# Performance work log

Hardware: AMD Instinct MI355X
Metric: run time of the kernel (lower is better)

## Reference

```python
import jax, jax.numpy as jnp
import numpy as np

B, T, N, D = 2, 10, 1024, 1024
NH = 16
HD = D // NH


def setup_inputs() -> dict:
    key = jax.random.key(0)
    ks = jax.random.split(key, 9)
    data = jax.random.normal(ks[0], (B, N, D), jnp.float32)
    traj_pos = jax.random.normal(ks[1], (B, T, N, 3), jnp.float32)
    q = jax.random.normal(ks[2], (B, T, N, 4), jnp.float32)
    traj_quat = q / (jnp.linalg.norm(q, axis=-1, keepdims=True) + 1e-10)
    certainty = jax.random.uniform(ks[3], (B, N), jnp.float32)
    s = 1.0 / np.sqrt(D).astype(np.float32)
    Wq = jax.random.normal(ks[4], (D, D), jnp.float32) * s
    Wk = jax.random.normal(ks[5], (D, D), jnp.float32) * s
    Wv = jax.random.normal(ks[6], (D, D), jnp.float32) * s
    Wo = jax.random.normal(ks[7], (D, D), jnp.float32) * s
    z = jnp.zeros((D,), jnp.float32)
    return {"data": data, "traj_pos": traj_pos, "traj_quat": traj_quat,
            "certainty": certainty, "Wq": Wq, "bq": z, "Wk": Wk, "bk": z,
            "Wv": Wv, "bv": z, "Wo": Wo, "bo": z}


def reference(data, traj_pos, traj_quat, certainty, Wq, bq, Wk, bk, Wv, bv, Wo, bo):
    b, n, d = data.shape
    # --- trajectory similarity scores (same for all batches: torch.mean over batch+time) ---
    # pos_dist[i,j] = mean_{b,t} ||p_bti - p_btj||
    pd = jnp.linalg.norm(traj_pos[:, :, :, None, :] - traj_pos[:, :, None, :, :], axis=-1).mean(axis=(0, 1))  # (n,n)
    qdm = jnp.linalg.norm(traj_quat[:, :, :, None, :] - traj_quat[:, :, None, :, :], axis=-1).mean(axis=(0, 1))
    qdp = jnp.linalg.norm(traj_quat[:, :, :, None, :] + traj_quat[:, :, None, :, :], axis=-1).mean(axis=(0, 1))
    qd = jnp.minimum(qdm, qdp)
    traj = jnp.exp(-pd - qd)
    traj = traj / traj.sum(axis=-1, keepdims=True)  # (n,n) row-normalized

    def proj(x, W, bias):
        return (x @ W.T + bias).reshape(b, n, NH, HD).transpose(0, 2, 1, 3)  # (b,h,n,hd)

    Q = proj(data, Wq, bq)
    K = proj(data, Wk, bk)
    V = proj(data, Wv, bv)
    scores = jnp.einsum('bhid,bhjd->bhij', Q, K) / np.sqrt(HD).astype(np.float32)
    combined = scores + 0.5 * traj[None, None]  # broadcast over (batch, heads)
    attn = jax.nn.softmax(combined, axis=-1)
    out = jnp.einsum('bhij,bhjd->bhid', attn, V).transpose(0, 2, 1, 3).reshape(b, n, d)
    out = out @ Wo.T + bo
    # certainty update from attention entropy
    avg_attn = attn.mean(axis=1)  # (b,n,n)
    p = jnp.clip(avg_attn, 1e-10, None)
    Hent = -jnp.sum(p * jnp.log(p), axis=-1)  # (b,n)
    H_max = np.log(n).astype(np.float32)
    new_certainty = jnp.maximum(certainty, jax.nn.sigmoid(H_max - Hent))
    return out, new_certainty
```

## Files before the change

### kernel.cpp

```cpp
#include <hip/hip_runtime.h>
#include <math.h>

#define NB 2
#define NN 1024
#define DD 1024
#define NHH 16
#define HDD 64
#define BTT 20

typedef unsigned short u16;
typedef short bf16x8 __attribute__((ext_vector_type(8)));
typedef float f32x4 __attribute__((ext_vector_type(4)));

#define HMAXL 6.93147180559945f
#define LN2 0.69314718055994531f
#define C1 0.18033688011112042f
#define TLC 0.72134752044448170f
#define KC  0.072134752044448170f
#define CH 520

#define TRAJ_OFF 0
#define TL_OFF    1048576
#define DATAB_OFF 1572864
#define WQB_OFF   2621440
#define WKB_OFF   3145728
#define WVB_OFF   3670016
#define WOB_OFF   4194304
#define QB_OFF    4718592
#define KB_OFF    5767168
#define VT_OFF    6815744
#define AOB_OFF   7864320
#define LV_OFF    8912896
#define RSP_OFF   8978432
#define EB_OFF    8982528

__device__ __forceinline__ float b2f(u16 h) { return __uint_as_float(((unsigned)h) << 16); }
__device__ __forceinline__ u16 f2bf(float f) {
  unsigned u = __float_as_uint(f);
  return (u16)((u + 0x7fffu + ((u >> 16) & 1u)) >> 16);
}
__device__ __forceinline__ unsigned pkbf(float a, float b) {
  unsigned r;
  asm("v_cvt_pk_bf16_f32 %0, %1, %2" : "=v"(r) : "v"(a), "v"(b));
  return r;
}
__device__ __forceinline__ void dma16(const void* g, void* l) {
  __builtin_amdgcn_global_load_lds((const __attribute__((address_space(1))) void*)g,
                                   (__attribute__((address_space(3))) void*)l, 16, 0, 0);
}

__global__ __launch_bounds__(256) void prep_kernel(const float* __restrict__ data,
                                                   const float* __restrict__ w0,
                                                   const float* __restrict__ w1,
                                                   const float* __restrict__ w2,
                                                   const float* __restrict__ w3,
                                                   u16* __restrict__ dd,
                                                   u16* __restrict__ d0, u16* __restrict__ d1,
                                                   u16* __restrict__ d2, u16* __restrict__ d3,
                                                   const float* __restrict__ pos,
                                                   const float* __restrict__ quat,
                                                   float* __restrict__ w,
                                                   float* __restrict__ rsp) {
  const int tid = threadIdx.x;
  const int bid = blockIdx.x;
  __shared__ float ld[8][BTT][8];
  __shared__ float wredS[4][8];
  if (bid >= 512) {
    int cb = bid - 512;
    int z = cb >> 10;
    const float* s;
    u16* d;
    size_t off = 0;
    if (z < 2) { s = data; d = dd; off = (size_t)z * 1048576; }
    else if (z == 2) { s = w0; d = d0; }
    else if (z == 3) { s = w1; d = d1; }
    else if (z == 4) { s = w2; d = d2; }
    else { s = w3; d = d3; }
    size_t i = off + (size_t)((cb & 1023) * 256 + tid) * 4;
    float4 v = *(const float4*)(s + i);
    ushort4 o = {f2bf(v.x), f2bf(v.y), f2bf(v.z), f2bf(v.w)};
    *(ushort4*)(d + i) = o;
    return;
  }
  const int jx = bid & 3;
  const int j = jx * 256 + tid;
  const int i0 = (bid >> 2) * 8;
  if (tid < 8 * BTT) {
    int ii = tid / BTT, bt = tid % BTT;
    const float* pp = pos + ((size_t)bt * NN + i0 + ii) * 3;
    ld[ii][bt][0] = pp[0]; ld[ii][bt][1] = pp[1]; ld[ii][bt][2] = pp[2];
    *(float4*)&ld[ii][bt][4] = *(const float4*)(quat + ((size_t)bt * NN + i0 + ii) * 4);
  }
  __syncthreads();
  float acc[8] = {};
  for (int bt = 0; bt < BTT; ++bt) {
    const float* pj = pos + ((size_t)bt * NN + j) * 3;
    float pjx = pj[0], pjy = pj[1], pjz = pj[2];
    float4 qj = *(const float4*)(quat + ((size_t)bt * NN + j) * 4);
#pragma unroll
    for (int ii = 0; ii < 8; ++ii) {
      float4 pi = *(const float4*)&ld[ii][bt][0];
      float4 qi = *(const float4*)&ld[ii][bt][4];
      float dx = pi.x - pjx, dy = pi.y - pjy, dz = pi.z - pjz;
      float d2 = fmaf(dz, dz, fmaf(dy, dy, dx * dx));
      float dot = fmaf(qi.w, qj.w, fmaf(qi.z, qj.z, fmaf(qi.y, qj.y, qi.x * qj.x)));
      float tq = fmaf(-2.f, fabsf(dot), 2.f);
      acc[ii] += sqrtf(d2) + sqrtf(fmaxf(tq, 0.f));
    }
  }
  const int wv = tid >> 6;
#pragma unroll
  for (int ii = 0; ii < 8; ++ii) {
    float v = exp2f(-acc[ii] * KC);
    w[(size_t)(i0 + ii) * NN + j] = v;
    float s = v;
#pragma unroll
    for (int off = 1; off < 64; off <<= 1) s += __shfl_xor(s, off, 64);
    if ((tid & 63) == 0) wredS[wv][ii] = s;
  }
  __syncthreads();
  if (tid < 8)
    rsp[jx * 1024 + i0 + tid] = wredS[0][tid] + wredS[1][tid] + wredS[2][tid] + wredS[3][tid];
}

__global__ __launch_bounds__(256, 3) void qkv_trajB_kernel(const u16* __restrict__ Ab,
                                                        const u16* __restrict__ Wq,
                                                        const u16* __restrict__ Wk,
                                                        const u16* __restrict__ Wv,
                                                        const float* __restrict__ bq,
                                                        const float* __restrict__ bk,
                                                        const float* __restrict__ bv,
                                                        u16* __restrict__ Qb,
                                                        u16* __restrict__ Kb,
                                                        u16* __restrict__ VtT,
                                                        const float* __restrict__ wtr,
                                                        const float* __restrict__ rsp,
                                                        u16* __restrict__ tl) {
  const int tid = threadIdx.x;
  __shared__ __align__(16) u16 As[128 * 64];
  __shared__ __align__(16) u16 Bs[2][64 * 64];
  if (blockIdx.x < 256) {
    int base = blockIdx.x * 4;
#pragma unroll
    for (int r = 0; r < 4; ++r) {
      int i = base + r;
      float inv = TLC / (rsp[i] + rsp[1024 + i] + rsp[2048 + i] + rsp[3072 + i]);
      float4 w4 = *(const float4*)(wtr + (size_t)i * NN + tid * 4);
      ushort4 o = {f2bf(w4.x * inv), f2bf(w4.y * inv), f2bf(w4.z * inv), f2bf(w4.w * inv)};
      *(ushort4*)(tl + (size_t)i * NN + tid * 4) = o;
    }
    return;
  }
  const int bid = blockIdx.x - 256;
  const bool isQK = bid < 256;
  const int rem = bid & 255;
  const int bn = (rem & 15) << 6;
  const int bm = (rem >> 4) << 7;
  const int w = tid >> 6, l = tid & 63, g = l >> 4, ln = l & 15;
  const int lr = l >> 3;
  const int sgc = ((l & 7) ^ lr) * 8;
  const u16* ApA = Ab + (size_t)(bm + w * 32 + lr) * DD + sgc;
  u16* dAc = As + (w * 4) * 512;
  const int mw = (w & 1) * 64, nw = (w >> 1) * 32;
  const int lx = ln & 7;
  f32x4 zero4 = {0.f, 0.f, 0.f, 0.f};
  if (isQK) {
    const u16* BqP = Wq + (size_t)(bn + w * 16 + lr) * DD + sgc;
    const u16* BkP = Wk + (size_t)(bn + w * 16 + lr) * DD + sgc;
    u16* dBq = Bs[0] + (w * 2) * 512;
    u16* dBk = Bs[1] + (w * 2) * 512;
    f32x4 acc[2][4][2];
#pragma unroll
    for (int z = 0; z < 2; ++z)
#pragma unroll
      for (int mt = 0; mt < 4; ++mt)
#pragma unroll
        for (int nt = 0; nt < 2; ++nt) acc[z][mt][nt] = zero4;
    for (int k0 = 0; k0 < DD; k0 += 64) {
      __syncthreads();
#pragma unroll
      for (int d = 0; d < 4; ++d)
        dma16(ApA + (size_t)(d * 8) * DD + k0, dAc + d * 512);
#pragma unroll
      for (int d = 0; d < 2; ++d) {
        dma16(BqP + (size_t)(d * 8) * DD + k0, dBq + d * 512);
        dma16(BkP + (size_t)(d * 8) * DD + k0, dBk + d * 512);
      }
      __syncthreads();
#pragma unroll
      for (int kc = 0; kc < 2; ++kc) {
        const int so = ((kc * 4 + g) ^ lx) * 8;
        bf16x8 afr[4], bqf[2], bkf[2];
#pragma unroll
        for (int nt = 0; nt < 2; ++nt) {
          int off = (nw + nt * 16 + ln) * 64 + so;
          bqf[nt] = *(const bf16x8*)&Bs[0][off];
          bkf[nt] = *(const bf16x8*)&Bs[1][off];
        }
#pragma unroll
        for (int mt = 0; mt < 4; ++mt)
          afr[mt] = *(const bf16x8*)&As[(mw + mt * 16 + ln) * 64 + so];
#pragma unroll
        for (int mt = 0; mt < 4; ++mt)
#pragma unroll
          for (int nt = 0; nt < 2; ++nt) {
            acc[0][mt][nt] = __builtin_amdgcn_mfma_f32_16x16x32_bf16(afr[mt], bqf[nt], acc[0][mt][nt], 0, 0, 0);
            acc[1][mt][nt] = __builtin_amdgcn_mfma_f32_16x16x32_bf16(afr[mt], bkf[nt], acc[1][mt][nt], 0, 0, 0);
          }
      }
    }
#pragma unroll
    for (int z = 0; z < 2; ++z) {
      u16* outp = z == 0 ? Qb : Kb;
      const float* bias = z == 0 ? bq : bk;
#pragma unroll
      for (int nt = 0; nt < 2; ++nt) {
        int n = bn + nw + nt * 16 + ln;
        float bb = bias[n];
#pragma unroll
        for (int mt = 0; mt < 4; ++mt) {
#pragma unroll
          for (int r = 0; r < 4; ++r) {
            int m = bm + mw + mt * 16 + g * 4 + r;
            outp[(size_t)m * DD + n] = f2bf(acc[z][mt][nt][r] + bb);
          }
        }
      }
    }
    return;
  }
  const u16* BvP = Wv + (size_t)(bn + w * 16 + lr) * DD + sgc;
  u16* dBv = Bs[0] + (w * 2) * 512;
  f32x4 acc[4][2];
#pragma unroll
  for (int mt = 0; mt < 4; ++mt)
#pragma unroll
    for (int nt = 0; nt < 2; ++nt) acc[mt][nt] = zero4;
  for (int k0 = 0; k0 < DD; k0 += 64) {
    __syncthreads();
#pragma unroll
    for (int d = 0; d < 4; ++d)
      dma16(ApA + (size_t)(d * 8) * DD + k0, dAc + d * 512);
#pragma unroll
    for (int d = 0; d < 2; ++d)
      dma16(BvP + (size_t)(d * 8) * DD + k0, dBv + d * 512);
    __syncthreads();
#pragma unroll
    for (int kc = 0; kc < 2; ++kc) {
      const int so = ((kc * 4 + g) ^ lx) * 8;
      bf16x8 bfr[2], afr[4];
#pragma unroll
      for (int nt = 0; nt < 2; ++nt)
        bfr[nt] = *(const bf16x8*)&Bs[0][(nw + nt * 16 + ln) * 64 + so];
#pragma unroll
      for (int mt = 0; mt < 4; ++mt)
        afr[mt] = *(const bf16x8*)&As[(mw + mt * 16 + ln) * 64 + so];
#pragma unroll
      for (int mt = 0; mt < 4; ++mt)
#pragma unroll
        for (int nt = 0; nt < 2; ++nt)
          acc[mt][nt] = __builtin_amdgcn_mfma_f32_16x16x32_bf16(afr[mt], bfr[nt], acc[mt][nt], 0, 0, 0);
    }
  }
#pragma unroll
  for (int nt = 0; nt < 2; ++nt) {
    int n = bn + nw + nt * 16 + ln;
    float bb = bv[n];
    int row = (((bm >> 10) << 4) + (n >> 6)) * 64 + (n & 63);
#pragma unroll
    for (int mt = 0; mt < 4; ++mt) {
      int tok = (bm & 1023) + mw + mt * 16 + g * 4;
      ushort4 pk = {f2bf(acc[mt][nt][0] + bb), f2bf(acc[mt][nt][1] + bb),
                    f2bf(acc[mt][nt][2] + bb), f2bf(acc[mt][nt][3] + bb)};
      *(ushort4*)(VtT + (size_t)row * NN + tok) = pk;
    }
  }
}

__global__ __launch_bounds__(256) void att_kernel(const u16* __restrict__ Qb,
                                                  const u16* __restrict__ Kb,
                                                  const u16* __restrict__ VtT,
                                                  const u16* __restrict__ tl,
                                                  u16* __restrict__ AOb,
                                                  float* __restrict__ Lv,
                                                  u16* __restrict__ Eb) {
  const int tid = threadIdx.x;
  const int bh = blockIdx.y;
  const int b = bh >> 4, h = bh & 15;
  const int i0 = blockIdx.x << 6;
  const int w = tid >> 6, l = tid & 63, g = l >> 4, ln = l & 15;
  const int wi0 = w * 16;
  __shared__ __align__(16) u16 Qs[8 * CH];
  __shared__ __align__(16) u16 Ks[2][8 * CH];
  __shared__ __align__(16) u16 Vts[2][8 * CH];
  __shared__ __align__(16) u16 Pt[64 * 72];
  __shared__ float lsc[64];
  const int c0 = 2 * w, c1 = 2 * w + 1;
  const int rr = 8 * (l >> 3);
  const int dcol = (l & 7) * 8;
  dma16(Qb + ((size_t)(b * NN) + i0 + c0 + rr) * DD + h * HDD + dcol, Qs + c0 * CH);
  dma16(Qb + ((size_t)(b * NN) + i0 + c1 + rr) * DD + h * HDD + dcol, Qs + c1 * CH);
  const int ig = i0 + wi0 + ln;
  u16* Erow = Eb + ((size_t)bh * NN + ig) * NN;
  const int lnlo = (ln & 7) * CH;
  const int lnhi = (ln >> 3) * 64;
  f32x4 zero4 = {0.f, 0.f, 0.f, 0.f};
  f32x4 oacc[4];
#pragma unroll
  for (int nt = 0; nt < 4; ++nt) oacc[nt] = zero4;
  float lacc = 0.f;
  for (int j0 = 0; j0 < NN; j0 += 128) {
    __syncthreads();
#pragma unroll
    for (int u = 0; u < 2; ++u) {
      int jb = j0 + u * 64;
      dma16(Kb + ((size_t)(b * NN) + jb + c0 + rr) * DD + h * HDD + dcol, Ks[u] + c0 * CH);
      dma16(Kb + ((size_t)(b * NN) + jb + c1 + rr) * DD + h * HDD + dcol, Ks[u] + c1 * CH);
      dma16(VtT + ((size_t)(bh * 64) + c0 + rr) * NN + jb + dcol, Vts[u] + c0 * CH);
      dma16(VtT + ((size_t)(bh * 64) + c1 + rr) * NN + jb + dcol, Vts[u] + c1 * CH);
    }
    ushort4 tlv[2][4];
#pragma unroll
    for (int u = 0; u < 2; ++u)
#pragma unroll
      for (int jt = 0; jt < 4; ++jt)
        tlv[u][jt] = *(const ushort4*)(tl + (size_t)ig * NN + j0 + u * 64 + jt * 16 + g * 4);
    __syncthreads();
    bf16x8 qf[2];
    qf[0] = *(const bf16x8*)&Qs[lnlo + (2 * w) * 64 + lnhi + g * 8];
    qf[1] = *(const bf16x8*)&Qs[lnlo + (2 * w) * 64 + lnhi + 32 + g * 8];
#pragma unroll
    for (int u = 0; u < 2; ++u) {
      f32x4 sacc[4];
      __builtin_amdgcn_s_setprio(1);
#pragma unroll
      for (int jt = 0; jt < 4; ++jt) {
        sacc[jt] = zero4;
#pragma unroll
        for (int kc = 0; kc < 2; ++kc) {
          bf16x8 af = *(const bf16x8*)&Ks[u][lnlo + (2 * jt) * 64 + lnhi + kc * 32 + g * 8];
          sacc[jt] = __builtin_amdgcn_mfma_f32_16x16x32_bf16(af, qf[kc], sacc[jt], 0, 0, 0);
        }
      }
      __builtin_amdgcn_s_setprio(0);
#pragma unroll
      for (int jt = 0; jt < 4; ++jt) {
        float e0 = exp2f(sacc[jt][0] * C1 + b2f(tlv[u][jt].x));
        float e1 = exp2f(sacc[jt][1] * C1 + b2f(tlv[u][jt].y));
        float e2 = exp2f(sacc[jt][2] * C1 + b2f(tlv[u][jt].z));
        float e3 = exp2f(sacc[jt][3] * C1 + b2f(tlv[u][jt].w));
        lacc += (e0 + e1) + (e2 + e3);
        uint2 pk = {pkbf(e0, e1), pkbf(e2, e3)};
        *(uint2*)(Pt + (wi0 + ln) * 72 + jt * 16 + g * 4) = pk;
        *(uint2*)(Erow + j0 + u * 64 + jt * 16 + g * 4) = pk;
      }
      bf16x8 pf[2];
      pf[0] = *(const bf16x8*)&Pt[(wi0 + ln) * 72 + g * 8];
      pf[1] = *(const bf16x8*)&Pt[(wi0 + ln) * 72 + 32 + g * 8];
      __builtin_amdgcn_s_setprio(1);
#pragma unroll
      for (int nt = 0; nt < 4; ++nt) {
#pragma unroll
        for (int kc = 0; kc < 2; ++kc) {
          bf16x8 vf = *(const bf16x8*)&Vts[u][lnlo + (2 * nt) * 64 + lnhi + kc * 32 + g * 8];
          oacc[nt] = __builtin_amdgcn_mfma_f32_16x16x32_bf16(pf[kc], vf, oacc[nt], 0, 0, 0);
        }
      }
      __builtin_amdgcn_s_setprio(0);
    }
  }
  lacc += __shfl_xor(lacc, 16, 64);
  lacc += __shfl_xor(lacc, 32, 64);
  if (g == 0) {
    Lv[(size_t)bh * NN + i0 + wi0 + ln] = lacc;
    lsc[wi0 + ln] = 1.f / lacc;
  }
  __syncthreads();
#pragma unroll
  for (int nt = 0; nt < 4; ++nt) {
    int d = nt * 16 + ln;
#pragma unroll
    for (int r = 0; r < 4; ++r) {
      int i = wi0 + g * 4 + r;
      float v = oacc[nt][r] * lsc[i];
      AOb[((size_t)(b * NN) + i0 + i) * DD + h * HDD + d] = f2bf(v);
    }
  }
}

__global__ __launch_bounds__(256) void gemmo_ent_kernel(const u16* __restrict__ Ab,
                                                        const u16* __restrict__ Wb,
                                                        const float* __restrict__ bias,
                                                        float* __restrict__ C,
                                                        const u16* __restrict__ Eb,
                                                        const float* __restrict__ Lv,
                                                        const float* __restrict__ cert,
                                                        float* __restrict__ outc) {
  const int tid = threadIdx.x;
  __shared__ __align__(16) u16 As[128 * 64];
  __shared__ __align__(16) u16 Bs[64 * 64];
  __shared__ float linvS[4][16];
  __shared__ float redS[4][4];
  if (blockIdx.x >= 256) {
    const int e = blockIdx.x - 256;
    const int b = e >> 8;
    const int ib4 = (e & 255) << 2;
    if (tid < 64) {
      int r = tid >> 4, h = tid & 15;
      linvS[r][h] = 1.f / Lv[((size_t)(b * 16 + h)) * NN + ib4 + r];
    }
    __syncthreads();
    const int jb = tid * 4;
    float A[4];
#pragma unroll
    for (int r = 0; r < 4; ++r) {
      float s0 = 0.f, s1 = 0.f, s2 = 0.f, s3 = 0.f;
#pragma unroll
      for (int h = 0; h < 16; ++h) {
        ushort4 v = *(const ushort4*)(Eb + (((size_t)(b * 16 + h)) * NN + ib4 + r) * NN + jb);
        float li = linvS[r][h];
        s0 = fmaf(b2f(v.x), li, s0); s1 = fmaf(b2f(v.y), li, s1);
        s2 = fmaf(b2f(v.z), li, s2); s3 = fmaf(b2f(v.w), li, s3);
      }
      float p0 = fmaxf(s0 * (1.f / NHH), 1e-10f);
      float p1 = fmaxf(s1 * (1.f / NHH), 1e-10f);
      float p2 = fmaxf(s2 * (1.f / NHH), 1e-10f);
      float p3 = fmaxf(s3 * (1.f / NHH), 1e-10f);
      A[r] = p0 * __log2f(p0) + p1 * __log2f(p1) + p2 * __log2f(p2) + p3 * __log2f(p3);
    }
#pragma unroll
    for (int r = 0; r < 4; ++r)
#pragma unroll
      for (int off = 1; off < 64; off <<= 1) A[r] += __shfl_xor(A[r], off, 64);
    const int wv = tid >> 6;
    if ((tid & 63) == 0) {
#pragma unroll
      for (int r = 0; r < 4; ++r) redS[wv][r] = A[r];
    }
    __syncthreads();
    if (tid < 4) {
      float H = -LN2 * (redS[0][tid] + redS[1][tid] + redS[2][tid] + redS[3][tid]);
      int idx = b * NN + ib4 + tid;
      float sg = 1.f / (1.f + expf(H - HMAXL));
      outc[idx] = fmaxf(cert[idx], sg);
    }
    return;
  }
  const int bn = (blockIdx.x & 15) << 6;
  const int bm = (blockIdx.x >> 4) << 7;
  const int w = tid >> 6, l = tid & 63, g = l >> 4, ln = l & 15;
  const int lr = l >> 3;
  const int sgc = ((l & 7) ^ lr) * 8;
  const u16* ApA = Ab + (size_t)(bm + w * 32 + lr) * DD + sgc;
  const u16* BoP = Wb + (size_t)(bn + w * 16 + lr) * DD + sgc;
  u16* dAc = As + (w * 4) * 512;
  u16* dBo = Bs + (w * 2) * 512;
  const int mw = (w & 1) * 64, nw = (w >> 1) * 32;
  const int lx = ln & 7;
  f32x4 zero4 = {0.f, 0.f, 0.f, 0.f};
  f32x4 acc[4][2];
#pragma unroll
  for (int mt = 0; mt < 4; ++mt)
#pragma unroll
    for (int nt = 0; nt < 2; ++nt) acc[mt][nt] = zero4;
  for (int k0 = 0; k0 < DD; k0 += 64) {
    __syncthreads();
#pragma unroll
    for (int d = 0; d < 4; ++d)
      dma16(ApA + (size_t)(d * 8) * DD + k0, dAc + d * 512);
#pragma unroll
    for (int d = 0; d < 2; ++d)
      dma16(BoP + (size_t)(d * 8) * DD + k0, dBo + d * 512);
    __syncthreads();
#pragma unroll
    for (int kc = 0; kc < 2; ++kc) {
      const int so = ((kc * 4 + g) ^ lx) * 8;
      bf16x8 bfr[2], afr[4];
#pragma unroll
      for (int nt = 0; nt < 2; ++nt)
        bfr[nt] = *(const bf16x8*)&Bs[(nw + nt * 16 + ln) * 64 + so];
#pragma unroll
      for (int mt = 0; mt < 4; ++mt)
        afr[mt] = *(const bf16x8*)&As[(mw + mt * 16 + ln) * 64 + so];
#pragma unroll
      for (int mt = 0; mt < 4; ++mt)
#pragma unroll
        for (int nt = 0; nt < 2; ++nt)
          acc[mt][nt] = __builtin_amdgcn_mfma_f32_16x16x32_bf16(afr[mt], bfr[nt], acc[mt][nt], 0, 0, 0);
    }
  }
#pragma unroll
  for (int nt = 0; nt < 2; ++nt) {
    int n = bn + nw + nt * 16 + ln;
    float bb = bias[n];
#pragma unroll
    for (int mt = 0; mt < 4; ++mt) {
#pragma unroll
      for (int r = 0; r < 4; ++r) {
        int m = bm + mw + mt * 16 + g * 4 + r;
        C[(size_t)m * DD + n] = acc[mt][nt][r] + bb;
      }
    }
  }
}

extern "C" void kernel_launch(void* const* d_in, const int* in_sizes, int n_in,
                              void* d_out, int out_size, void* d_ws, size_t ws_size,
                              hipStream_t stream) {
  const float* data      = (const float*)d_in[0];
  const float* traj_pos  = (const float*)d_in[1];
  const float* traj_quat = (const float*)d_in[2];
  const float* certainty = (const float*)d_in[3];
  const float* Wq = (const float*)d_in[4];
  const float* bq = (const float*)d_in[5];
  const float* Wk = (const float*)d_in[6];
  const float* bk = (const float*)d_in[7];
  const float* Wv = (const float*)d_in[8];
  const float* bv = (const float*)d_in[9];
  const float* Wo = (const float*)d_in[10];
  const float* bo = (const float*)d_in[11];

  float* ws = (float*)d_ws;
  float* wtr  = ws + TRAJ_OFF;
  u16* tl    = (u16*)(ws + TL_OFF);
  u16* datab = (u16*)(ws + DATAB_OFF);
  u16* wqb   = (u16*)(ws + WQB_OFF);
  u16* wkb   = (u16*)(ws + WKB_OFF);
  u16* wvb   = (u16*)(ws + WVB_OFF);
  u16* wob   = (u16*)(ws + WOB_OFF);
  u16* Qb    = (u16*)(ws + QB_OFF);
  u16* Kb    = (u16*)(ws + KB_OFF);
  u16* VtT   = (u16*)(ws + VT_OFF);
  u16* AOb   = (u16*)(ws + AOB_OFF);
  float* Lv   = ws + LV_OFF;
  float* rsp  = ws + RSP_OFF;
  u16* Eb    = (u16*)(ws + EB_OFF);
  float* out  = (float*)d_out;
  float* outc = out + (size_t)NB * NN * DD;

  prep_kernel<<<6656, 256, 0, stream>>>(data, Wq, Wk, Wv, Wo,
                                        datab, wqb, wkb, wvb, wob,
                                        traj_pos, traj_quat, wtr, rsp);
  qkv_trajB_kernel<<<768, 256, 0, stream>>>(datab, wqb, wkb, wvb, bq, bk, bv,
                                            Qb, Kb, VtT, wtr, rsp, tl);
  att_kernel<<<dim3(NN / 64, NB * NHH), 256, 0, stream>>>(Qb, Kb, VtT, tl, AOb, Lv, Eb);
  gemmo_ent_kernel<<<768, 256, 0, stream>>>(AOb, wob, bo, out, Eb, Lv, certainty, outc);
}
```

Before: 193.5 us.

## Load attention Q/K/V fragments directly from global memory instead of LDS staging

Removes the shared-memory staging of Q, K and V^T tiles (async dma16 copies plus two block barriers per 128-key step) in the attention kernel. Each wave now reads its MFMA operand fragments straight from global memory and processes 64 keys per iteration with no __syncthreads. This drops the barriers and LDS traffic, and the smaller LDS footprint may allow higher occupancy. In exchange, the four waves of a block each fetch the same K/V data separately, relying on L1/L2 hits, and the loads are less coalesced and no longer prefetched ahead of the compute.

```diff
diff --git a/kernel.cpp b/kernel.cpp
--- a/kernel.cpp
+++ b/kernel.cpp
@@ -17,7 +17,6 @@
 #define C1 0.18033688011112042f
 #define TLC 0.72134752044448170f
 #define KC  0.072134752044448170f
-#define CH 520
 
 #define TRAJ_OFF 0
 #define TL_OFF    1048576
@@ -290,84 +289,64 @@
   const int i0 = blockIdx.x << 6;
   const int w = tid >> 6, l = tid & 63, g = l >> 4, ln = l & 15;
   const int wi0 = w * 16;
-  __shared__ __align__(16) u16 Qs[8 * CH];
-  __shared__ __align__(16) u16 Ks[2][8 * CH];
-  __shared__ __align__(16) u16 Vts[2][8 * CH];
   __shared__ __align__(16) u16 Pt[64 * 72];
   __shared__ float lsc[64];
-  const int c0 = 2 * w, c1 = 2 * w + 1;
-  const int rr = 8 * (l >> 3);
-  const int dcol = (l & 7) * 8;
-  dma16(Qb + ((size_t)(b * NN) + i0 + c0 + rr) * DD + h * HDD + dcol, Qs + c0 * CH);
-  dma16(Qb + ((size_t)(b * NN) + i0 + c1 + rr) * DD + h * HDD + dcol, Qs + c1 * CH);
+  const int rlo = ln & 7;
+  const int rhi = 8 * (ln >> 3);
   const int ig = i0 + wi0 + ln;
   u16* Erow = Eb + ((size_t)bh * NN + ig) * NN;
-  const int lnlo = (ln & 7) * CH;
-  const int lnhi = (ln >> 3) * 64;
+  const u16* Qrow = Qb + ((size_t)(b * NN) + i0 + 16 * w + rlo + rhi) * DD + h * HDD;
+  bf16x8 qf[2];
+  qf[0] = *(const bf16x8*)(Qrow + g * 8);
+  qf[1] = *(const bf16x8*)(Qrow + 32 + g * 8);
+  const u16* Kbase = Kb + ((size_t)(b * NN) + rlo + rhi) * DD + h * HDD;
+  const u16* Vbase = VtT + ((size_t)(bh * 64) + rlo + rhi) * NN;
   f32x4 zero4 = {0.f, 0.f, 0.f, 0.f};
   f32x4 oacc[4];
 #pragma unroll
   for (int nt = 0; nt < 4; ++nt) oacc[nt] = zero4;
   float lacc = 0.f;
-  for (int j0 = 0; j0 < NN; j0 += 128) {
-    __syncthreads();
-#pragma unroll
-    for (int u = 0; u < 2; ++u) {
-      int jb = j0 + u * 64;
-      dma16(Kb + ((size_t)(b * NN) + jb + c0 + rr) * DD + h * HDD + dcol, Ks[u] + c0 * CH);
-      dma16(Kb + ((size_t)(b * NN) + jb + c1 + rr) * DD + h * HDD + dcol, Ks[u] + c1 * CH);
-      dma16(VtT + ((size_t)(bh * 64) + c0 + rr) * NN + jb + dcol, Vts[u] + c0 * CH);
-      dma16(VtT + ((size_t)(bh * 64) + c1 + rr) * NN + jb + dcol, Vts[u] + c1 * CH);
-    }
-    ushort4 tlv[2][4];
-#pragma unroll
-    for (int u = 0; u < 2; ++u)
-#pragma unroll
-      for (int jt = 0; jt < 4; ++jt)
-        tlv[u][jt] = *(const ushort4*)(tl + (size_t)ig * NN + j0 + u * 64 + jt * 16 + g * 4);
-    __syncthreads();
-    bf16x8 qf[2];
-    qf[0] = *(const bf16x8*)&Qs[lnlo + (2 * w) * 64 + lnhi + g * 8];
-    qf[1] = *(const bf16x8*)&Qs[lnlo + (2 * w) * 64 + lnhi + 32 + g * 8];
-#pragma unroll
-    for (int u = 0; u < 2; ++u) {
-      f32x4 sacc[4];
-      __builtin_amdgcn_s_setprio(1);
-#pragma unroll
-      for (int jt = 0; jt < 4; ++jt) {
-        sacc[jt] = zero4;
-#pragma unroll
-        for (int kc = 0; kc < 2; ++kc) {
-          bf16x8 af = *(const bf16x8*)&Ks[u][lnlo + (2 * jt) * 64 + lnhi + kc * 32 + g * 8];
-          sacc[jt] = __builtin_amdgcn_mfma_f32_16x16x32_bf16(af, qf[kc], sacc[jt], 0, 0, 0);
-        }
-      }
-      __builtin_amdgcn_s_setprio(0);
-#pragma unroll
-      for (int jt = 0; jt < 4; ++jt) {
-        float e0 = exp2f(sacc[jt][0] * C1 + b2f(tlv[u][jt].x));
-        float e1 = exp2f(sacc[jt][1] * C1 + b2f(tlv[u][jt].y));
-        float e2 = exp2f(sacc[jt][2] * C1 + b2f(tlv[u][jt].z));
-        float e3 = exp2f(sacc[jt][3] * C1 + b2f(tlv[u][jt].w));
-        lacc += (e0 + e1) + (e2 + e3);
-        uint2 pk = {pkbf(e0, e1), pkbf(e2, e3)};
-        *(uint2*)(Pt + (wi0 + ln) * 72 + jt * 16 + g * 4) = pk;
-        *(uint2*)(Erow + j0 + u * 64 + jt * 16 + g * 4) = pk;
-      }
-      bf16x8 pf[2];
-      pf[0] = *(const bf16x8*)&Pt[(wi0 + ln) * 72 + g * 8];
-      pf[1] = *(const bf16x8*)&Pt[(wi0 + ln) * 72 + 32 + g * 8];
-      __builtin_amdgcn_s_setprio(1);
-#pragma unroll
-      for (int nt = 0; nt < 4; ++nt) {
-#pragma unroll
-        for (int kc = 0; kc < 2; ++kc) {
-          bf16x8 vf = *(const bf16x8*)&Vts[u][lnlo + (2 * nt) * 64 + lnhi + kc * 32 + g * 8];
-          oacc[nt] = __builtin_amdgcn_mfma_f32_16x16x32_bf16(pf[kc], vf, oacc[nt], 0, 0, 0);
-        }
-      }
-      __builtin_amdgcn_s_setprio(0);
-    }
+  for (int jb = 0; jb < NN; jb += 64) {
+    ushort4 tlv[4];
+#pragma unroll
+    for (int jt = 0; jt < 4; ++jt)
+      tlv[jt] = *(const ushort4*)(tl + (size_t)ig * NN + jb + jt * 16 + g * 4);
+    f32x4 sacc[4];
+    __builtin_amdgcn_s_setprio(1);
+#pragma unroll
+    for (int jt = 0; jt < 4; ++jt) {
+      sacc[jt] = zero4;
+#pragma unroll
+      for (int kc = 0; kc < 2; ++kc) {
+        bf16x8 af = *(const bf16x8*)(Kbase + (size_t)(jb + 16 * jt) * DD + kc * 32 + g * 8);
+        sacc[jt] = __builtin_amdgcn_mfma_f32_16x16x32_bf16(af, qf[kc], sacc[jt], 0, 0, 0);
+      }
+    }
+    __builtin_amdgcn_s_setprio(0);
+#pragma unroll
+    for (int jt = 0; jt < 4; ++jt) {
+      float e0 = exp2f(sacc[jt][0] * C1 + b2f(tlv[jt].x));
+      float e1 = exp2f(sacc[jt][1] * C1 + b2f(tlv[jt].y));
+      float e2 = exp2f(sacc[jt][2] * C1 + b2f(tlv[jt].z));
+      float e3 = exp2f(sacc[jt][3] * C1 + b2f(tlv[jt].w));
+      lacc += (e0 + e1) + (e2 + e3);
+      uint2 pk = {pkbf(e0, e1), pkbf(e2, e3)};
+      *(uint2*)(Pt + (wi0 + ln) * 72 + jt * 16 + g * 4) = pk;
+      *(uint2*)(Erow + jb + jt * 16 + g * 4) = pk;
+    }
+    bf16x8 pf[2];
+    pf[0] = *(const bf16x8*)&Pt[(wi0 + ln) * 72 + g * 8];
+    pf[1] = *(const bf16x8*)&Pt[(wi0 + ln) * 72 + 32 + g * 8];
+    __builtin_amdgcn_s_setprio(1);
+#pragma unroll
+    for (int nt = 0; nt < 4; ++nt) {
+#pragma unroll
+      for (int kc = 0; kc < 2; ++kc) {
+        bf16x8 vf = *(const bf16x8*)(Vbase + (size_t)(16 * nt) * NN + jb + kc * 32 + g * 8);
+        oacc[nt] = __builtin_amdgcn_mfma_f32_16x16x32_bf16(pf[kc], vf, oacc[nt], 0, 0, 0);
+      }
+    }
+    __builtin_amdgcn_s_setprio(0);
   }
   lacc += __shfl_xor(lacc, 16, 64);
   lacc += __shfl_xor(lacc, 32, 64);
```

Result: slower. 235.6 us (+21.8%).
